# Kernel tuning notes

Measured on AMD Instinct MI355X. Metric: run time of the kernel, lower is better.

Reference implementation:

```python
import jax, jax.numpy as jnp
import numpy as np

POOL = (7, 7)


def crop_and_resize(fmap, boxes, box_idx, ph, pw):
    """tf.image.crop_and_resize (bilinear) for normalized boxes (y1,x1,y2,x2).
    fmap: [B,H,W,C], boxes: [N,4], box_idx: [N] int32 -> [N,ph,pw,C]."""
    H, W = fmap.shape[1], fmap.shape[2]
    dt = fmap.dtype
    y1, x1, y2, x2 = boxes[:, 0], boxes[:, 1], boxes[:, 2], boxes[:, 3]
    ty = jnp.arange(ph, dtype=dt) / (ph - 1)
    tx = jnp.arange(pw, dtype=dt) / (pw - 1)
    ys = (y1[:, None] + ty[None, :] * (y2 - y1)[:, None]) * (H - 1)  # [N,ph]
    xs = (x1[:, None] + tx[None, :] * (x2 - x1)[:, None]) * (W - 1)  # [N,pw]
    y0f = jnp.clip(jnp.floor(ys), 0.0, H - 1)
    x0f = jnp.clip(jnp.floor(xs), 0.0, W - 1)
    y0 = y0f.astype(jnp.int32)
    x0 = x0f.astype(jnp.int32)
    y1i = jnp.minimum(y0 + 1, H - 1)
    x1i = jnp.minimum(x0 + 1, W - 1)
    wy = (ys - y0f)[:, :, None, None]  # [N,ph,1,1]
    wx = (xs - x0f)[:, None, :, None]  # [N,1,pw,1]
    b = box_idx[:, None, None]
    v00 = fmap[b, y0[:, :, None], x0[:, None, :]]  # [N,ph,pw,C]
    v01 = fmap[b, y0[:, :, None], x1i[:, None, :]]
    v10 = fmap[b, y1i[:, :, None], x0[:, None, :]]
    v11 = fmap[b, y1i[:, :, None], x1i[:, None, :]]
    top = v00 + (v01 - v00) * wx
    bot = v10 + (v11 - v10) * wx
    return top + (bot - top) * wy


def setup_inputs() -> dict:
    key = jax.random.key(0)
    k1, k2, k3, k4, kp2, kp3, kp4, kp5 = jax.random.split(key, 8)
    B, N, C = 1, 1000, 256
    y1 = jax.random.uniform(k1, (B, N)) * 0.7
    x1 = jax.random.uniform(k2, (B, N)) * 0.7
    h = jax.random.uniform(k3, (B, N)) * 0.4 + 0.01
    w = jax.random.uniform(k4, (B, N)) * 0.4 + 0.01
    ROIboxes = jnp.stack([y1, x1, jnp.minimum(y1 + h, 1.0), jnp.minimum(x1 + w, 1.0)], axis=-1)
    meta = np.zeros((B, 93), np.float32)
    meta[:, 4:7] = [1024.0, 1024.0, 3.0]  # image_shape
    return {
        "ROIboxes": ROIboxes.astype(jnp.float32),
        "image_meta": jnp.asarray(meta),
        "P2": jax.random.normal(kp2, (B, 256, 256, C), jnp.float32),
        "P3": jax.random.normal(kp3, (B, 128, 128, C), jnp.float32),
        "P4": jax.random.normal(kp4, (B, 64, 64, C), jnp.float32),
        "P5": jax.random.normal(kp5, (B, 32, 32, C), jnp.float32),
    }


def reference(ROIboxes, image_meta, P2, P3, P4, P5):
    feature_maps = [P2, P3, P4, P5]
    B, N = ROIboxes.shape[0], ROIboxes.shape[1]
    boxes = jax.lax.stop_gradient(ROIboxes.reshape(-1, 4))  # [B*N,4]
    box_idx = jnp.repeat(jnp.arange(B, dtype=jnp.int32), N)
    image_shape = image_meta[0, 4:7]
    image_area = image_shape[0] * image_shape[1]
    h = boxes[:, 2] - boxes[:, 0]
    w = boxes[:, 3] - boxes[:, 1]
    roi_level = jnp.log2(jnp.sqrt(h * w) / (224.0 / jnp.sqrt(image_area)))
    roi_level = jnp.clip(4 + jnp.round(roi_level).astype(jnp.int32), 2, 5)  # [B*N]
    ph, pw = POOL
    C = P2.shape[-1]
    pooled = jnp.zeros((B * N, ph, pw, C), P2.dtype)
    for i, level in enumerate(range(2, 6)):
        p = crop_and_resize(feature_maps[i], boxes, box_idx, ph, pw)
        mask = (roi_level == level)[:, None, None, None]
        pooled = pooled + jnp.where(mask, p, 0.0)
    # Original gathers per-level then sorts back to original ROI order; the
    # masked-sum above produces the same per-ROI result in original order.
    return pooled[None]  # [1, B*N, ph, pw, C]
```

## Files before the change

### kernel.cpp

```cpp
#include <hip/hip_runtime.h>
#include <hip/hip_bf16.h>
#include <math.h>


#define CCH 256
#define PH 7
#define PW 7

__global__ __launch_bounds__(256) void PyramidROIAlign_kernel(
    const float* __restrict__ boxes,
    const float* __restrict__ meta,
    const float* __restrict__ P2,
    const float* __restrict__ P3,
    const float* __restrict__ P4,
    const float* __restrict__ P5,
    float* __restrict__ out,
    int total_boxes,
    int n_per_batch)
{
    int idx = blockIdx.x * blockDim.x + threadIdx.x;
    int c4 = (idx & 63) << 2;
    int p  = idx >> 6;
    if (p >= total_boxes * (PH * PW)) return;

    int n  = p / (PH * PW);
    int r  = p - n * (PH * PW);
    int py = r / PW;
    int px = r - py * PW;

    float y1 = boxes[n * 4 + 0];
    float x1 = boxes[n * 4 + 1];
    float y2 = boxes[n * 4 + 2];
    float x2 = boxes[n * 4 + 3];
    float h = y2 - y1;
    float w = x2 - x1;

    float area  = meta[4] * meta[5];
    float scale = 224.0f / sqrtf(area);
    float lvlf  = log2f(sqrtf(h * w) / scale);
    int level = 4 + (int)rintf(lvlf);
    level = min(max(level, 2), 5);

    const float* fmap;
    int H;
    switch (level) {
        case 2:  fmap = P2; H = 256; break;
        case 3:  fmap = P3; H = 128; break;
        case 4:  fmap = P4; H = 64;  break;
        default: fmap = P5; H = 32;  break;
    }
    int W = H;
    int b = n / n_per_batch;
    fmap += (size_t)b * H * W * CCH;

    float ty = (float)py / (float)(PH - 1);
    float tx = (float)px / (float)(PW - 1);
    float ys = (y1 + ty * (y2 - y1)) * (float)(H - 1);
    float xs = (x1 + tx * (x2 - x1)) * (float)(W - 1);

    float y0f = fminf(fmaxf(floorf(ys), 0.0f), (float)(H - 1));
    float x0f = fminf(fmaxf(floorf(xs), 0.0f), (float)(W - 1));
    int y0 = (int)y0f;
    int x0 = (int)x0f;
    int y1i = min(y0 + 1, H - 1);
    int x1i = min(x0 + 1, W - 1);
    float wy = ys - y0f;
    float wx = xs - x0f;

    const float4* r00 = (const float4*)(fmap + ((size_t)y0  * W + x0 ) * CCH + c4);
    const float4* r01 = (const float4*)(fmap + ((size_t)y0  * W + x1i) * CCH + c4);
    const float4* r10 = (const float4*)(fmap + ((size_t)y1i * W + x0 ) * CCH + c4);
    const float4* r11 = (const float4*)(fmap + ((size_t)y1i * W + x1i) * CCH + c4);

    float4 v00 = *r00;
    float4 v01 = *r01;
    float4 v10 = *r10;
    float4 v11 = *r11;

    float4 o;
    {
        float top = v00.x + (v01.x - v00.x) * wx;
        float bot = v10.x + (v11.x - v10.x) * wx;
        o.x = top + (bot - top) * wy;
        top = v00.y + (v01.y - v00.y) * wx;
        bot = v10.y + (v11.y - v10.y) * wx;
        o.y = top + (bot - top) * wy;
        top = v00.z + (v01.z - v00.z) * wx;
        bot = v10.z + (v11.z - v10.z) * wx;
        o.z = top + (bot - top) * wy;
        top = v00.w + (v01.w - v00.w) * wx;
        bot = v10.w + (v11.w - v10.w) * wx;
        o.w = top + (bot - top) * wy;
    }

    *((float4*)(out + (size_t)p * CCH + c4)) = o;
}

extern "C" void kernel_launch(void* const* d_in, const int* in_sizes, int n_in,
                              void* d_out, int out_size, void* d_ws, size_t ws_size,
                              hipStream_t stream) {
    const float* boxes = (const float*)d_in[0];
    const float* meta  = (const float*)d_in[1];
    const float* P2    = (const float*)d_in[2];
    const float* P3    = (const float*)d_in[3];
    const float* P4    = (const float*)d_in[4];
    const float* P5    = (const float*)d_in[5];
    float* out = (float*)d_out;

    int total_boxes = in_sizes[0] / 4;
    int B = in_sizes[1] / 93;
    if (B < 1) B = 1;
    int n_per_batch = total_boxes / B;

    long total_threads = (long)total_boxes * (PH * PW) * 64;
    int threads = 256;
    int blocks = (int)((total_threads + threads - 1) / threads);

    PyramidROIAlign_kernel<<<blocks, threads, 0, stream>>>(
        boxes, meta, P2, P3, P4, P5, out, total_boxes, n_per_batch);
}
```

Measured before the change: 31.82 us.

## Assign one wavefront per output row and loop over pooled columns

Each 64-lane wavefront now handles a whole pooled row (7 output pixels) instead of one pixel, so box loading, level selection and y-interpolation setup are computed once per row rather than per pixel. The row index is made wave-uniform with readfirstlane so the box and level math can run on scalar registers. The launch uses seven times fewer threads, and each thread issues more loads in an unrolled loop. This lowers parallelism in exchange for less redundant per-pixel setup.

```diff
diff --git a/kernel.cpp b/kernel.cpp
--- a/kernel.cpp
+++ b/kernel.cpp
@@ -18,26 +18,22 @@
     int total_boxes,
     int n_per_batch)
 {
-    int idx = blockIdx.x * blockDim.x + threadIdx.x;
-    int c4 = (idx & 63) << 2;
-    int p  = idx >> 6;
-    if (p >= total_boxes * (PH * PW)) return;
+    int wid  = (blockIdx.x * blockDim.x + threadIdx.x) >> 6;
+    int lane = threadIdx.x & 63;
+    if (wid >= total_boxes * PH) return;
+    wid = __builtin_amdgcn_readfirstlane(wid);
 
-    int n  = p / (PH * PW);
-    int r  = p - n * (PH * PW);
-    int py = r / PW;
-    int px = r - py * PW;
+    int n  = wid / PH;
+    int py = wid - n * PH;
 
     float y1 = boxes[n * 4 + 0];
     float x1 = boxes[n * 4 + 1];
     float y2 = boxes[n * 4 + 2];
     float x2 = boxes[n * 4 + 3];
-    float h = y2 - y1;
-    float w = x2 - x1;
 
     float area  = meta[4] * meta[5];
     float scale = 224.0f / sqrtf(area);
-    float lvlf  = log2f(sqrtf(h * w) / scale);
+    float lvlf  = log2f(sqrtf((y2 - y1) * (x2 - x1)) / scale);
     int level = 4 + (int)rintf(lvlf);
     level = min(max(level, 2), 5);
 
@@ -53,34 +49,39 @@
     int b = n / n_per_batch;
     fmap += (size_t)b * H * W * CCH;
 
-    float ty = (float)py / (float)(PH - 1);
-    float tx = (float)px / (float)(PW - 1);
-    float ys = (y1 + ty * (y2 - y1)) * (float)(H - 1);
-    float xs = (x1 + tx * (x2 - x1)) * (float)(W - 1);
+    float ty  = (float)py / (float)(PH - 1);
+    float ys  = (y1 + ty * (y2 - y1)) * (float)(H - 1);
+    float y0f = fminf(fmaxf(floorf(ys), 0.0f), (float)(H - 1));
+    int   y0  = (int)y0f;
+    int   y1r = min(y0 + 1, H - 1);
+    float wy  = ys - y0f;
 
-    float y0f = fminf(fmaxf(floorf(ys), 0.0f), (float)(H - 1));
-    float x0f = fminf(fmaxf(floorf(xs), 0.0f), (float)(W - 1));
-    int y0 = (int)y0f;
-    int x0 = (int)x0f;
-    int y1i = min(y0 + 1, H - 1);
-    int x1i = min(x0 + 1, W - 1);
-    float wy = ys - y0f;
-    float wx = xs - x0f;
+    const float* row0 = fmap + (size_t)y0  * W * CCH;
+    const float* row1 = fmap + (size_t)y1r * W * CCH;
 
-    const float4* r00 = (const float4*)(fmap + ((size_t)y0  * W + x0 ) * CCH + c4);
-    const float4* r01 = (const float4*)(fmap + ((size_t)y0  * W + x1i) * CCH + c4);
-    const float4* r10 = (const float4*)(fmap + ((size_t)y1i * W + x0 ) * CCH + c4);
-    const float4* r11 = (const float4*)(fmap + ((size_t)y1i * W + x1i) * CCH + c4);
+    int c = lane << 2;
+    float* optr = out + ((size_t)wid * PW) * CCH + c;
 
-    float4 v00 = *r00;
-    float4 v01 = *r01;
-    float4 v10 = *r10;
-    float4 v11 = *r11;
+    #pragma unroll
+    for (int px = 0; px < PW; ++px) {
+        float tx  = (float)px / (float)(PW - 1);
+        float xs  = (x1 + tx * (x2 - x1)) * (float)(W - 1);
+        float x0f = fminf(fmaxf(floorf(xs), 0.0f), (float)(W - 1));
+        int   x0  = (int)x0f;
+        int   x1r = min(x0 + 1, W - 1);
+        float wx  = xs - x0f;
 
-    float4 o;
-    {
-        float top = v00.x + (v01.x - v00.x) * wx;
-        float bot = v10.x + (v11.x - v10.x) * wx;
+        int o0 = x0  * CCH + c;
+        int o1 = x1r * CCH + c;
+        float4 v00 = *(const float4*)(row0 + o0);
+        float4 v01 = *(const float4*)(row0 + o1);
+        float4 v10 = *(const float4*)(row1 + o0);
+        float4 v11 = *(const float4*)(row1 + o1);
+
+        float4 o;
+        float top, bot;
+        top = v00.x + (v01.x - v00.x) * wx;
+        bot = v10.x + (v11.x - v10.x) * wx;
         o.x = top + (bot - top) * wy;
         top = v00.y + (v01.y - v00.y) * wx;
         bot = v10.y + (v11.y - v10.y) * wx;
@@ -91,9 +92,9 @@
         top = v00.w + (v01.w - v00.w) * wx;
         bot = v10.w + (v11.w - v10.w) * wx;
         o.w = top + (bot - top) * wy;
+
+        *((float4*)(optr + px * CCH)) = o;
     }
-
-    *((float4*)(out + (size_t)p * CCH + c4)) = o;
 }
 
 extern "C" void kernel_launch(void* const* d_in, const int* in_sizes, int n_in,
@@ -112,7 +113,7 @@
     if (B < 1) B = 1;
     int n_per_batch = total_boxes / B;
 
-    long total_threads = (long)total_boxes * (PH * PW) * 64;
+    long total_threads = (long)total_boxes * PH * 64;
     int threads = 256;
     int blocks = (int)((total_threads + threads - 1) / threads);
 
```

Result: faster. 29.76 us (-6.5%).
